# Kernel optimization log

Measured on AMD Instinct MI355X. Metric: run time of the kernel, lower is better.

Reference implementation:

```python
import jax, jax.numpy as jnp
import numpy as np

# Dimensions matching init_kwargs
O = 4096   # out_features
I = 4096   # in_features
R = 32     # svd_rank
G = 64     # n_groups
GS = I // G  # group_size = 64
NBITS = 4
NUM_BYTES = O * I * NBITS // 8


def setup_inputs() -> dict:
    key = jax.random.key(0)
    ks = jax.random.split(key, 7)
    return {
        "x": jax.random.normal(ks[0], (1, 4096, I), dtype=jnp.float32),
        # bit-packed int4 weights, two nibbles per byte (stored as int32 holding 0..255)
        "w_packed": jax.random.randint(ks[1], (NUM_BYTES,), 0, 256, dtype=jnp.int32),
        "svd_up": jax.random.normal(ks[2], (O, R), dtype=jnp.float32) * 0.02,
        "svd_down": jax.random.normal(ks[3], (R, I), dtype=jnp.float32) * 0.02,
        "scale": jax.random.uniform(ks[4], (O, G, 1), dtype=jnp.float32, minval=0.001, maxval=0.02),
        "zero_point": jax.random.uniform(ks[5], (O, G, 1), dtype=jnp.float32, minval=0.0, maxval=15.0),
        "bias": jax.random.normal(ks[6], (O,), dtype=jnp.float32) * 0.01,
    }


def _dequantize(w_packed, svd_up, svd_down, scale, zero_point):
    # Unpack two 4-bit values per byte (low nibble first).
    low = w_packed & 0xF
    high = (w_packed >> 4) & 0xF
    w_q = jnp.stack([low, high], axis=-1).reshape(O, G, GS).astype(jnp.float32)
    # Per-group affine dequant: (q - zero) * scale, then SVD low-rank correction.
    W = ((w_q - zero_point) * scale).reshape(O, I)
    return W + svd_up @ svd_down  # [O, I]


def reference(x, w_packed, svd_up, svd_down, scale, zero_point, bias):
    # forward_int8 path (tokens > 16, int8_matmul=True)
    W_f = _dequantize(w_packed, svd_up, svd_down, scale, zero_point).T  # [I, O]
    xm = x.reshape(-1, I)  # [N, I]
    # Dynamic per-row activation quant
    scale_x = jnp.max(jnp.abs(xm), axis=1, keepdims=True) / 127.0  # [N, 1]
    x_q = jnp.clip(jnp.round(xm / scale_x), -128, 127).astype(jnp.int8)
    # Dynamic per-column weight quant
    scale_w = jnp.max(jnp.abs(W_f), axis=0, keepdims=True) / 127.0  # [1, O]
    W_q = jnp.clip(jnp.round(W_f / scale_w), -128, 127).astype(jnp.int8)
    # int8 GEMM with int32 accumulation, then dequant scales + bias
    acc = jnp.matmul(x_q.astype(jnp.int32), W_q.astype(jnp.int32))  # [N, O] int32
    out = acc.astype(jnp.float32) * scale_x * scale_w + bias
    return out.reshape(*x.shape[:-1], O)
```

## Files before the change

### kernel.cpp

```cpp
#include <hip/hip_runtime.h>
#include <cstdint>
#include <cstddef>

#define I_DIM 4096
#define O_DIM 4096
#define RNK 32
#define NGRP 64
#define N_TOK 4096

typedef int v4i  __attribute__((ext_vector_type(4)));
typedef int v16i __attribute__((ext_vector_type(16)));

__device__ __forceinline__ int clamp_i8(float v) {
    int q = (int)rintf(v);
    q = q < -128 ? -128 : q;
    q = q > 127 ? 127 : q;
    return q;
}

#define BO 4

__global__ __launch_bounds__(256) void quant_w_kernel(
    const int* __restrict__ w_packed, const float* __restrict__ svd_up,
    const float* __restrict__ svd_down, const float* __restrict__ scale,
    const float* __restrict__ zp, char* __restrict__ w_q,
    float* __restrict__ scale_w)
{
    __shared__ float s_sc[BO][NGRP];
    __shared__ float s_zp[BO][NGRP];
    __shared__ float s_up[RNK][BO];
    __shared__ float s_red[BO][4];
    __shared__ float s_sw[BO];

    const int tid = threadIdx.x;
    const int o0 = blockIdx.x * BO;

    if (tid < RNK * BO) {
        const int r = tid >> 2, ro = tid & 3;
        s_up[r][ro] = svd_up[(size_t)(o0 + ro) * RNK + r];
    }
    for (int t = tid; t < BO * NGRP; t += 256) {
        s_sc[t >> 6][t & 63] = scale[(size_t)(o0 + (t >> 6)) * NGRP + (t & 63)];
        s_zp[t >> 6][t & 63] = zp[(size_t)(o0 + (t >> 6)) * NGRP + (t & 63)];
    }
    __syncthreads();

    float W[4][BO][4];

#pragma unroll
    for (int jq = 0; jq < 4; jq++) {
        const int q = tid + 256 * jq;
        const int g = q >> 4;
#pragma unroll
        for (int ro = 0; ro < BO; ro++) {
            const int2 b2 = *(const int2*)&w_packed[(size_t)(o0 + ro) * (I_DIM / 2) + 2 * q];
            const float sc = s_sc[ro][g], z = s_zp[ro][g];
            W[jq][ro][0] = ((float)(b2.x & 0xF) - z) * sc;
            W[jq][ro][1] = ((float)((b2.x >> 4) & 0xF) - z) * sc;
            W[jq][ro][2] = ((float)(b2.y & 0xF) - z) * sc;
            W[jq][ro][3] = ((float)((b2.y >> 4) & 0xF) - z) * sc;
        }
    }

#pragma unroll 2
    for (int r = 0; r < RNK; r++) {
        const float4* dr = (const float4*)(svd_down + (size_t)r * I_DIM);
        float u[BO];
#pragma unroll
        for (int ro = 0; ro < BO; ro++) u[ro] = s_up[r][ro];
        float4 d[4];
#pragma unroll
        for (int jq = 0; jq < 4; jq++) d[jq] = dr[tid + 256 * jq];
#pragma unroll
        for (int jq = 0; jq < 4; jq++) {
#pragma unroll
            for (int ro = 0; ro < BO; ro++) {
                W[jq][ro][0] += u[ro] * d[jq].x;
                W[jq][ro][1] += u[ro] * d[jq].y;
                W[jq][ro][2] += u[ro] * d[jq].z;
                W[jq][ro][3] += u[ro] * d[jq].w;
            }
        }
    }

    float vmax[BO];
#pragma unroll
    for (int ro = 0; ro < BO; ro++) vmax[ro] = 0.0f;
#pragma unroll
    for (int jq = 0; jq < 4; jq++)
#pragma unroll
        for (int ro = 0; ro < BO; ro++)
            vmax[ro] = fmaxf(vmax[ro],
                fmaxf(fmaxf(fabsf(W[jq][ro][0]), fabsf(W[jq][ro][1])),
                      fmaxf(fabsf(W[jq][ro][2]), fabsf(W[jq][ro][3]))));

    const int lane = tid & 63, wv = tid >> 6;
#pragma unroll
    for (int ro = 0; ro < BO; ro++) {
        float m = vmax[ro];
        for (int off = 32; off > 0; off >>= 1)
            m = fmaxf(m, __shfl_down(m, off, 64));
        if (lane == 0) s_red[ro][wv] = m;
    }
    __syncthreads();
    if (tid < BO) {
        const float m = fmaxf(fmaxf(s_red[tid][0], s_red[tid][1]),
                              fmaxf(s_red[tid][2], s_red[tid][3]));
        const float sw = m / 127.0f;
        scale_w[o0 + tid] = sw;
        s_sw[tid] = sw;
    }
    __syncthreads();

    float inv[BO];
#pragma unroll
    for (int ro = 0; ro < BO; ro++) inv[ro] = 1.0f / s_sw[ro];

#pragma unroll
    for (int jq = 0; jq < 4; jq++) {
        const int q = tid + 256 * jq;
#pragma unroll
        for (int ro = 0; ro < BO; ro++) {
            const int q0 = clamp_i8(W[jq][ro][0] * inv[ro]);
            const int q1 = clamp_i8(W[jq][ro][1] * inv[ro]);
            const int q2 = clamp_i8(W[jq][ro][2] * inv[ro]);
            const int q3 = clamp_i8(W[jq][ro][3] * inv[ro]);
            ((int*)w_q)[(size_t)(o0 + ro) * (I_DIM / 4) + q] =
                (q0 & 0xFF) | ((q1 & 0xFF) << 8) | ((q2 & 0xFF) << 16) | ((q3 & 0xFF) << 24);
        }
    }
}

__global__ __launch_bounds__(256) void quant_x_kernel(
    const float* __restrict__ x, char* __restrict__ x_q,
    float* __restrict__ scale_x)
{
    const int n = blockIdx.x;
    const int tid = threadIdx.x;
    const float4* xr = (const float4*)(x + (size_t)n * I_DIM);
    float4 v[4];
    float m = 0.0f;
#pragma unroll
    for (int j = 0; j < 4; j++) {
        v[j] = xr[tid + 256 * j];
        m = fmaxf(m, fmaxf(fmaxf(fabsf(v[j].x), fabsf(v[j].y)),
                           fmaxf(fabsf(v[j].z), fabsf(v[j].w))));
    }
    __shared__ float s_red[4];
    __shared__ float s_sx;
    for (int off = 32; off > 0; off >>= 1)
        m = fmaxf(m, __shfl_down(m, off, 64));
    if ((tid & 63) == 0) s_red[tid >> 6] = m;
    __syncthreads();
    if (tid == 0) {
        const float mm = fmaxf(fmaxf(s_red[0], s_red[1]),
                               fmaxf(s_red[2], s_red[3]));
        const float sx = mm / 127.0f;
        scale_x[n] = sx;
        s_sx = sx;
    }
    __syncthreads();
    const float sx = s_sx;
    int* outw = (int*)(x_q + (size_t)n * I_DIM);
#pragma unroll
    for (int j = 0; j < 4; j++) {
        const int q0 = clamp_i8(v[j].x / sx);
        const int q1 = clamp_i8(v[j].y / sx);
        const int q2 = clamp_i8(v[j].z / sx);
        const int q3 = clamp_i8(v[j].w / sx);
        outw[tid + 256 * j] =
            (q0 & 0xFF) | ((q1 & 0xFF) << 8) | ((q2 & 0xFF) << 16) | ((q3 & 0xFF) << 24);
    }
}

#define BM 128
#define BN 128
#define BK 128

__global__ __launch_bounds__(256) void gemm_i8_kernel(
    const char* __restrict__ x_q, const char* __restrict__ w_q,
    const float* __restrict__ scale_x, const float* __restrict__ scale_w,
    const float* __restrict__ bias, float* __restrict__ out)
{
    __shared__ v4i As4[BM * BK / 16];
    __shared__ v4i Bs4[BN * BK / 16];
    char* As = (char*)As4;
    char* Bs = (char*)Bs4;

    const int tid = threadIdx.x;
    const int bm0 = blockIdx.x * BM;
    const int bn0 = blockIdx.y * BN;
    const int lane = tid & 63, wv = tid >> 6;
    const int wm = wv & 1, wn = wv >> 1;
    const int l31 = lane & 31, h = lane >> 5;

    v16i acc[2][2];
#pragma unroll
    for (int mt = 0; mt < 2; mt++)
#pragma unroll
        for (int nt = 0; nt < 2; nt++)
            acc[mt][nt] = (v16i)(0);

    for (int kk = 0; kk < I_DIM / BK; kk++) {
        const int k0 = kk * BK;
#pragma unroll
        for (int j = 0; j < 4; j++) {
            const int c = tid + 256 * j;
            const int row = c >> 3;
            const int kc = (c & 7) ^ (row & 7);
            const char* ga = x_q + (size_t)(bm0 + row) * I_DIM + k0 + kc * 16;
            __builtin_amdgcn_global_load_lds(
                (const __attribute__((address_space(1))) unsigned int*)ga,
                (__attribute__((address_space(3))) unsigned int*)(As + c * 16),
                16, 0, 0);
            const char* gb = w_q + (size_t)(bn0 + row) * I_DIM + k0 + kc * 16;
            __builtin_amdgcn_global_load_lds(
                (const __attribute__((address_space(1))) unsigned int*)gb,
                (__attribute__((address_space(3))) unsigned int*)(Bs + c * 16),
                16, 0, 0);
        }
        __syncthreads();
#pragma unroll
        for (int s = 0; s < 4; s++) {
            v4i af[2], bf[2];
#pragma unroll
            for (int mt = 0; mt < 2; mt++) {
                const int row = wm * 64 + mt * 32 + l31;
                const int kc = (s * 2 + h) ^ (row & 7);
                af[mt] = *(const v4i*)(As + row * BK + kc * 16);
            }
#pragma unroll
            for (int nt = 0; nt < 2; nt++) {
                const int row = wn * 64 + nt * 32 + l31;
                const int kc = (s * 2 + h) ^ (row & 7);
                bf[nt] = *(const v4i*)(Bs + row * BK + kc * 16);
            }
#pragma unroll
            for (int mt = 0; mt < 2; mt++)
#pragma unroll
                for (int nt = 0; nt < 2; nt++)
                    acc[mt][nt] = __builtin_amdgcn_mfma_i32_32x32x32_i8(
                        af[mt], bf[nt], acc[mt][nt], 0, 0, 0);
        }
        __syncthreads();
    }

#pragma unroll
    for (int mt = 0; mt < 2; mt++) {
        const int rbase = bm0 + wm * 64 + mt * 32 + 4 * h;
        float sx[16];
#pragma unroll
        for (int reg = 0; reg < 16; reg++)
            sx[reg] = scale_x[rbase + (reg & 3) + 8 * (reg >> 2)];
#pragma unroll
        for (int nt = 0; nt < 2; nt++) {
            const int oc = bn0 + wn * 64 + nt * 32 + l31;
            const float sw = scale_w[oc];
            const float bs = bias[oc];
#pragma unroll
            for (int reg = 0; reg < 16; reg++) {
                const int rr = rbase + (reg & 3) + 8 * (reg >> 2);
                out[(size_t)rr * O_DIM + oc] =
                    (float)acc[mt][nt][reg] * sx[reg] * sw + bs;
            }
        }
    }
}

extern "C" void kernel_launch(void* const* d_in, const int* in_sizes, int n_in,
                              void* d_out, int out_size, void* d_ws, size_t ws_size,
                              hipStream_t stream) {
    const float* x        = (const float*)d_in[0];
    const int*   w_packed = (const int*)d_in[1];
    const float* svd_up   = (const float*)d_in[2];
    const float* svd_down = (const float*)d_in[3];
    const float* scale    = (const float*)d_in[4];
    const float* zp       = (const float*)d_in[5];
    const float* bias     = (const float*)d_in[6];
    float* out = (float*)d_out;

    char* ws = (char*)d_ws;
    char*  w_q     = ws;
    char*  x_q     = ws + ((size_t)16 << 20);
    float* scale_w = (float*)(ws + ((size_t)32 << 20));
    float* scale_x = (float*)(ws + ((size_t)32 << 20) + 16384);

    quant_w_kernel<<<O_DIM / BO, 256, 0, stream>>>(w_packed, svd_up, svd_down,
                                                   scale, zp, w_q, scale_w);
    quant_x_kernel<<<N_TOK, 256, 0, stream>>>(x, x_q, scale_x);
    gemm_i8_kernel<<<dim3(N_TOK / BM, O_DIM / BN), 256, 0, stream>>>(
        x_q, w_q, scale_x, scale_w, bias, out);
}
```

Before: 263.3 us.

## Fuse activation and weight quantization into one launch, restructure SVD loop

Merges the x-quantization and weight-dequant/quantization kernels into a single launch whose blocks split by blockIdx, which removes one kernel launch and lets the two independent jobs overlap on the GPU. The SVD correction loop now runs inside each column chunk, reading svd_up straight from global memory instead of staging it in shared memory, and the abs-max is computed per chunk. It also adds a launch-bounds occupancy hint of 4 blocks. The price is branch divergence between block types, plus more global and scalar loads of svd_down and svd_up per chunk, since svd_down is now reloaded per r for each jq.

```diff
diff --git a/kernel.cpp b/kernel.cpp
--- a/kernel.cpp
+++ b/kernel.cpp
@@ -20,25 +20,62 @@
 
 #define BO 4
 
-__global__ __launch_bounds__(256) void quant_w_kernel(
+__global__ __launch_bounds__(256, 4) void quant_fused_kernel(
+    const float* __restrict__ x, char* __restrict__ x_q,
+    float* __restrict__ scale_x,
     const int* __restrict__ w_packed, const float* __restrict__ svd_up,
     const float* __restrict__ svd_down, const float* __restrict__ scale,
     const float* __restrict__ zp, char* __restrict__ w_q,
     float* __restrict__ scale_w)
 {
+    const int tid = threadIdx.x;
+
+    if (blockIdx.x < N_TOK) {
+        const int n = blockIdx.x;
+        const float4* xr = (const float4*)(x + (size_t)n * I_DIM);
+        float4 v[4];
+        float m = 0.0f;
+#pragma unroll
+        for (int j = 0; j < 4; j++) {
+            v[j] = xr[tid + 256 * j];
+            m = fmaxf(m, fmaxf(fmaxf(fabsf(v[j].x), fabsf(v[j].y)),
+                               fmaxf(fabsf(v[j].z), fabsf(v[j].w))));
+        }
+        __shared__ float sx_red[4];
+        __shared__ float s_sx;
+        for (int off = 32; off > 0; off >>= 1)
+            m = fmaxf(m, __shfl_down(m, off, 64));
+        if ((tid & 63) == 0) sx_red[tid >> 6] = m;
+        __syncthreads();
+        if (tid == 0) {
+            const float mm = fmaxf(fmaxf(sx_red[0], sx_red[1]),
+                                   fmaxf(sx_red[2], sx_red[3]));
+            const float sx = mm / 127.0f;
+            scale_x[n] = sx;
+            s_sx = sx;
+        }
+        __syncthreads();
+        const float sx = s_sx;
+        int* outw = (int*)(x_q + (size_t)n * I_DIM);
+#pragma unroll
+        for (int j = 0; j < 4; j++) {
+            const int q0 = clamp_i8(v[j].x / sx);
+            const int q1 = clamp_i8(v[j].y / sx);
+            const int q2 = clamp_i8(v[j].z / sx);
+            const int q3 = clamp_i8(v[j].w / sx);
+            outw[tid + 256 * j] =
+                (q0 & 0xFF) | ((q1 & 0xFF) << 8) | ((q2 & 0xFF) << 16) | ((q3 & 0xFF) << 24);
+        }
+        return;
+    }
+
+    const int o0 = (blockIdx.x - N_TOK) * BO;
+
     __shared__ float s_sc[BO][NGRP];
     __shared__ float s_zp[BO][NGRP];
-    __shared__ float s_up[RNK][BO];
     __shared__ float s_red[BO][4];
     __shared__ float s_sw[BO];
 
-    const int tid = threadIdx.x;
-    const int o0 = blockIdx.x * BO;
-
-    if (tid < RNK * BO) {
-        const int r = tid >> 2, ro = tid & 3;
-        s_up[r][ro] = svd_up[(size_t)(o0 + ro) * RNK + r];
-    }
     for (int t = tid; t < BO * NGRP; t += 256) {
         s_sc[t >> 6][t & 63] = scale[(size_t)(o0 + (t >> 6)) * NGRP + (t & 63)];
         s_zp[t >> 6][t & 63] = zp[(size_t)(o0 + (t >> 6)) * NGRP + (t & 63)];
@@ -46,11 +83,16 @@
     __syncthreads();
 
     float W[4][BO][4];
+    float vmax[BO];
+#pragma unroll
+    for (int ro = 0; ro < BO; ro++) vmax[ro] = 0.0f;
 
 #pragma unroll
     for (int jq = 0; jq < 4; jq++) {
         const int q = tid + 256 * jq;
+        const int i = 4 * q;
         const int g = q >> 4;
+
 #pragma unroll
         for (int ro = 0; ro < BO; ro++) {
             const int2 b2 = *(const int2*)&w_packed[(size_t)(o0 + ro) * (I_DIM / 2) + 2 * q];
@@ -60,39 +102,27 @@
             W[jq][ro][2] = ((float)(b2.y & 0xF) - z) * sc;
             W[jq][ro][3] = ((float)((b2.y >> 4) & 0xF) - z) * sc;
         }
-    }
-
-#pragma unroll 2
-    for (int r = 0; r < RNK; r++) {
-        const float4* dr = (const float4*)(svd_down + (size_t)r * I_DIM);
-        float u[BO];
-#pragma unroll
-        for (int ro = 0; ro < BO; ro++) u[ro] = s_up[r][ro];
-        float4 d[4];
-#pragma unroll
-        for (int jq = 0; jq < 4; jq++) d[jq] = dr[tid + 256 * jq];
-#pragma unroll
-        for (int jq = 0; jq < 4; jq++) {
+
+#pragma unroll 4
+        for (int r = 0; r < RNK; r++) {
+            const float4 d = *(const float4*)&svd_down[(size_t)r * I_DIM + i];
 #pragma unroll
             for (int ro = 0; ro < BO; ro++) {
-                W[jq][ro][0] += u[ro] * d[jq].x;
-                W[jq][ro][1] += u[ro] * d[jq].y;
-                W[jq][ro][2] += u[ro] * d[jq].z;
-                W[jq][ro][3] += u[ro] * d[jq].w;
-            }
-        }
-    }
-
-    float vmax[BO];
-#pragma unroll
-    for (int ro = 0; ro < BO; ro++) vmax[ro] = 0.0f;
-#pragma unroll
-    for (int jq = 0; jq < 4; jq++)
-#pragma unroll
-        for (int ro = 0; ro < BO; ro++)
+                const float u = svd_up[(size_t)(o0 + ro) * RNK + r];
+                W[jq][ro][0] += u * d.x;
+                W[jq][ro][1] += u * d.y;
+                W[jq][ro][2] += u * d.z;
+                W[jq][ro][3] += u * d.w;
+            }
+        }
+
+#pragma unroll
+        for (int ro = 0; ro < BO; ro++) {
             vmax[ro] = fmaxf(vmax[ro],
                 fmaxf(fmaxf(fabsf(W[jq][ro][0]), fabsf(W[jq][ro][1])),
                       fmaxf(fabsf(W[jq][ro][2]), fabsf(W[jq][ro][3]))));
+        }
+    }
 
     const int lane = tid & 63, wv = tid >> 6;
 #pragma unroll
@@ -128,48 +158,6 @@
             ((int*)w_q)[(size_t)(o0 + ro) * (I_DIM / 4) + q] =
                 (q0 & 0xFF) | ((q1 & 0xFF) << 8) | ((q2 & 0xFF) << 16) | ((q3 & 0xFF) << 24);
         }
-    }
-}
-
-__global__ __launch_bounds__(256) void quant_x_kernel(
-    const float* __restrict__ x, char* __restrict__ x_q,
-    float* __restrict__ scale_x)
-{
-    const int n = blockIdx.x;
-    const int tid = threadIdx.x;
-    const float4* xr = (const float4*)(x + (size_t)n * I_DIM);
-    float4 v[4];
-    float m = 0.0f;
-#pragma unroll
-    for (int j = 0; j < 4; j++) {
-        v[j] = xr[tid + 256 * j];
-        m = fmaxf(m, fmaxf(fmaxf(fabsf(v[j].x), fabsf(v[j].y)),
-                           fmaxf(fabsf(v[j].z), fabsf(v[j].w))));
-    }
-    __shared__ float s_red[4];
-    __shared__ float s_sx;
-    for (int off = 32; off > 0; off >>= 1)
-        m = fmaxf(m, __shfl_down(m, off, 64));
-    if ((tid & 63) == 0) s_red[tid >> 6] = m;
-    __syncthreads();
-    if (tid == 0) {
-        const float mm = fmaxf(fmaxf(s_red[0], s_red[1]),
-                               fmaxf(s_red[2], s_red[3]));
-        const float sx = mm / 127.0f;
-        scale_x[n] = sx;
-        s_sx = sx;
-    }
-    __syncthreads();
-    const float sx = s_sx;
-    int* outw = (int*)(x_q + (size_t)n * I_DIM);
-#pragma unroll
-    for (int j = 0; j < 4; j++) {
-        const int q0 = clamp_i8(v[j].x / sx);
-        const int q1 = clamp_i8(v[j].y / sx);
-        const int q2 = clamp_i8(v[j].z / sx);
-        const int q3 = clamp_i8(v[j].w / sx);
-        outw[tid + 256 * j] =
-            (q0 & 0xFF) | ((q1 & 0xFF) << 8) | ((q2 & 0xFF) << 16) | ((q3 & 0xFF) << 24);
     }
 }
 
@@ -285,9 +273,8 @@
     float* scale_w = (float*)(ws + ((size_t)32 << 20));
     float* scale_x = (float*)(ws + ((size_t)32 << 20) + 16384);
 
-    quant_w_kernel<<<O_DIM / BO, 256, 0, stream>>>(w_packed, svd_up, svd_down,
-                                                   scale, zp, w_q, scale_w);
-    quant_x_kernel<<<N_TOK, 256, 0, stream>>>(x, x_q, scale_x);
+    quant_fused_kernel<<<N_TOK + O_DIM / BO, 256, 0, stream>>>(
+        x, x_q, scale_x, w_packed, svd_up, svd_down, scale, zp, w_q, scale_w);
     gemm_i8_kernel<<<dim3(N_TOK / BM, O_DIM / BN), 256, 0, stream>>>(
         x_q, w_q, scale_x, scale_w, bias, out);
 }
```

New measurement: 256.3 us. 2.7% less time.
